# Optimization experiments

Hardware: AMD Instinct MI355X
Metric: run time of the kernel (lower is better)

The kernel has to match this reference:

```python
import jax, jax.numpy as jnp
import numpy as np

BN_EPS = 1e-5

def setup_inputs() -> dict:
    key = jax.random.key(0)
    k_x, k_w, k_g, k_b, k_p = jax.random.split(key, 5)
    N, Cin, H, W = 32, 128, 56, 56
    Cout, K = 256, 3
    x = jax.random.normal(k_x, (N, Cin, H, W), dtype=jnp.float32)
    # random spatial permutation (Dconv_rand's torch.randperm(H*W))
    perm = jax.random.permutation(k_p, H * W).astype(jnp.int32)
    # conv weight, kaiming-ish scale
    w = jax.random.normal(k_w, (Cout, Cin, K, K), dtype=jnp.float32) * (2.0 / (Cin * K * K)) ** 0.5
    gamma = jnp.ones((Cout,), dtype=jnp.float32)
    beta = jnp.zeros((Cout,), dtype=jnp.float32)
    return {"x": x, "w": w, "gamma": gamma, "beta": beta, "perm": perm}


def reference(x, w, gamma, beta, perm):
    N, C, H, W = x.shape
    # Dconv_rand: randomly permute spatial positions, then standard 3x3 conv
    xp = x.reshape(N, C, H * W)[:, :, perm].reshape(N, C, H, W)
    y = jax.lax.conv_general_dilated(
        xp, w,
        window_strides=(1, 1),
        padding=((1, 1), (1, 1)),
        dimension_numbers=("NCHW", "OIHW", "NCHW"),
    )  # [N, Cout, H, W]
    # BatchNorm2d (training-mode batch stats, biased variance, eps=1e-5)
    mean = jnp.mean(y, axis=(0, 2, 3), keepdims=True)
    var = jnp.mean((y - mean) ** 2, axis=(0, 2, 3), keepdims=True)
    y_hat = (y - mean) * jax.lax.rsqrt(var + BN_EPS)
    out = y_hat * gamma.reshape(1, -1, 1, 1) + beta.reshape(1, -1, 1, 1)
    return jnp.maximum(out, 0.0)  # ReLU
```

## Files before the change

kernel.cpp:

```cpp
#include <hip/hip_runtime.h>
#include <hip/hip_bf16.h>
#include <stdint.h>

typedef __attribute__((ext_vector_type(8))) short bf16x8;
typedef __attribute__((ext_vector_type(4))) float f32x4;

#define N_IMG 32
#define CIN 128
#define COUT 256
#define HH 56
#define HW (HH*HH)
#define HP 58
#define PXTOT (N_IMG*HW)
#define NT 36

#define XP_BYTES    27557888u
#define WT_BYTES    589824u
#define INV_BYTES   12544u
#define STATS_BYTES 2048u
#define WS_MIN      (XP_BYTES + WT_BYTES + INV_BYTES + STATS_BYTES)
#define Y_BYTES     51380224u

__device__ __forceinline__ unsigned short f2bf(float f) {
  unsigned int u = __builtin_bit_cast(unsigned int, f);
  unsigned int r = u + 0x7FFFu + ((u >> 16) & 1u);
  return (unsigned short)(r >> 16);
}
__device__ __forceinline__ float bf2f(unsigned short s) {
  return __builtin_bit_cast(float, (unsigned int)s << 16);
}
__device__ __forceinline__ void gload_lds16(const void* g, void* l) {
  __builtin_amdgcn_global_load_lds((const __attribute__((address_space(1))) void*)g,
                                   (__attribute__((address_space(3))) void*)l, 16, 0, 0);
}

#define BAR()    __builtin_amdgcn_s_barrier()
#define WAITV4() asm volatile("s_waitcnt vmcnt(4)" ::: "memory")
#define WAITV0() asm volatile("s_waitcnt vmcnt(0)" ::: "memory")
#define WAITL()  asm volatile("s_waitcnt lgkmcnt(0)" ::: "memory")
#define SCHEDB() __builtin_amdgcn_sched_barrier(0)

__global__ __launch_bounds__(256) void wcvt_kernel(const float* __restrict__ w,
                                                   unsigned short* __restrict__ wt,
                                                   const int* __restrict__ perm,
                                                   int* __restrict__ inv,
                                                   float* __restrict__ stats) {
  int i = blockIdx.x * 256 + threadIdx.x;
  if (i < HW) inv[perm[i]] = i;
  if (i < 512) stats[i] = 0.f;
  if (i >= NT * COUT * 32) return;
  int kk = i >> 13;
  int r = i & 8191;
  int co = r >> 5, cl = r & 31;
  int o = kk >> 2, cb = kk & 3;
  int c = cb * 32 + cl;
  wt[i] = f2bf(w[(co * CIN + c) * 9 + o]);
}

__global__ __launch_bounds__(256) void pad_perm_kernel(const float* __restrict__ x,
                                                       const int* __restrict__ inv,
                                                       unsigned short* __restrict__ xp) {
  __shared__ unsigned short T[64 * 128];
  __shared__ int dest_off[64];
  int b = blockIdx.x;
  int n = b / 49;
  int k = b % 49;
  int s0 = k * 64;
  int t = threadIdx.x;

  if (t < 160) {
    int pi = k * 5 + (t >> 5);
    if (pi < 228) {
      int h, w2;
      if (pi < 58)       { h = 0;            w2 = pi; }
      else if (pi < 116) { h = 57;           w2 = pi - 58; }
      else if (pi < 172) { h = pi - 116 + 1; w2 = 0; }
      else               { h = pi - 172 + 1; w2 = 57; }
      uint2 z = {0u, 0u};
      *(uint2*)(xp + (size_t)((n * HP + h) * HP + w2) * CIN + (t & 31) * 4) = z;
    }
  }

  if (t < 64) {
    int s = inv[s0 + t];
    int h = s / HH, w = s % HH;
    dest_off[t] = ((n * HP + h + 1) * HP + (w + 1)) * CIN;
  }
  const float* xplane = x + (size_t)n * CIN * HW;
  #pragma unroll
  for (int i = 0; i < 32; ++i) {
    int idx = i * 256 + t;
    int c = idx >> 6, j = idx & 63;
    float v = xplane[c * HW + s0 + j];
    int byte = j * 256 + ((2 * c) ^ ((j & 7) << 4));
    *(unsigned short*)((char*)T + byte) = f2bf(v);
  }
  __syncthreads();
  #pragma unroll
  for (int i = 0; i < 4; ++i) {
    int u = i * 256 + t;
    int j = u >> 4, chunk = u & 15;
    int byte = j * 256 + ((chunk * 16) ^ ((j & 7) << 4));
    bf16x8 v = *(const bf16x8*)((const char*)T + byte);
    *(bf16x8*)(xp + dest_off[j] + chunk * 8) = v;
  }
}

template<int YMODE>
__global__ __launch_bounds__(256, 2) void conv_kernel(const unsigned short* __restrict__ xp,
                                                      const unsigned short* __restrict__ wt,
                                                      unsigned short* __restrict__ ybf,
                                                      float* __restrict__ yf32,
                                                      float* __restrict__ stats) {
  extern __shared__ unsigned short lds[];
  int t = threadIdx.x;
  int lane = t & 63, wid = t >> 6;
  int l = lane & 15, g = lane >> 4;
  int phys = blockIdx.x;
  int b = (phys & 7) * 98 + (phys >> 3);
  int pT = b >> 1;
  int coT = b & 1;
  int p0 = pT * 256;

  int lg = ((lane & 3) - (lane >> 3)) & 3;
  int aoff[2], adst[2];
  #pragma unroll
  for (int i = 0; i < 2; ++i) {
    int r = (wid * 2 + i) * 16 + (lane >> 2);
    aoff[i] = r * 32 + lg * 8;
    adst[i] = (wid * 2 + i) * 512 + lane * 8;
  }
  int bsrc[4], bdst[4];
  #pragma unroll
  for (int i = 0; i < 4; ++i) {
    int r = (wid * 4 + i) * 16 + (lane >> 2);
    int px = p0 + r;
    int n = px / HW, s = px % HW;
    int hi = s / HH, wi = s % HH;
    bsrc[i] = ((n * HP + hi) * HP + wi) * CIN + lg * 8;
    bdst[i] = (wid * 4 + i) * 512 + lane * 8;
  }
  const unsigned short* wbase = wt + coT * 128 * 32;

  auto stageA = [&](int kt) {
    const unsigned short* s0 = wbase + kt * 8192;
    unsigned short* d = lds + (kt & 1) * 4096;
    gload_lds16(s0 + aoff[0], d + adst[0]);
    gload_lds16(s0 + aoff[1], d + adst[1]);
  };
  auto stageB = [&](int kt, int buf) {
    int o = kt >> 2, cb = kt & 3;
    int koff = ((o / 3) * HP + (o % 3)) * CIN + cb * 32;
    unsigned short* d = lds + 8192 + buf * 8192;
    #pragma unroll
    for (int i = 0; i < 4; ++i)
      gload_lds16(xp + bsrc[i] + koff, d + bdst[i]);
  };

  int pcs = ((g + (l >> 1)) & 3) * 8;
  int arow = l * 32 + pcs;
  int brow = (wid * 64 + l) * 32 + pcs;

  bf16x8 afr[8], bfr[4];
  f32x4 acc[8][4];
  #pragma unroll
  for (int m = 0; m < 8; ++m)
    #pragma unroll
    for (int n = 0; n < 4; ++n) acc[m][n] = (f32x4)0.f;

#define LDA_ALL { _Pragma("unroll") for (int mm = 0; mm < 8; ++mm) \
    afr[mm] = *(const bf16x8*)(curA + arow + mm * 16 * 32); }
#define LDB_ALL { _Pragma("unroll") for (int nn = 0; nn < 4; ++nn) \
    bfr[nn] = *(const bf16x8*)(curB + brow + nn * 16 * 32); }
#define MFMA_ALL { _Pragma("unroll") for (int mm = 0; mm < 8; ++mm) \
    _Pragma("unroll") for (int nn = 0; nn < 4; ++nn) \
      acc[mm][nn] = __builtin_amdgcn_mfma_f32_16x16x32_bf16(afr[mm], bfr[nn], acc[mm][nn], 0, 0, 0); }

  stageA(0);
  stageB(0, 0);
  stageB(1, 1);
  WAITV4();
  BAR();

  int pb = 0;
  #pragma unroll 1
  for (int kt = 0; kt < NT; ++kt) {
    const unsigned short* curA = lds + (kt & 1) * 4096;
    const unsigned short* curB = lds + 8192 + pb * 8192;
    bool st1 = (kt + 1) < NT;
    bool st2 = (kt + 2) < NT;
    int pb2 = pb + 2; if (pb2 >= 3) pb2 -= 3;
    LDA_ALL; LDB_ALL;
    if (st1) stageA(kt + 1);
    if (st2) stageB(kt + 2, pb2);
    BAR();
    WAITL(); SCHEDB();
    __builtin_amdgcn_s_setprio(1);
    MFMA_ALL;
    __builtin_amdgcn_s_setprio(0);
    if (st2) { WAITV4(); } else if (st1) { WAITV0(); }
    BAR();
    pb = (pb + 1 == 3) ? 0 : pb + 1;
  }
#undef LDA_ALL
#undef LDB_ALL
#undef MFMA_ALL

  float ps1[8][4], ps2[8][4];
  #pragma unroll
  for (int m = 0; m < 8; ++m)
    #pragma unroll
    for (int j = 0; j < 4; ++j) {
      float a = 0.f, b2 = 0.f;
      #pragma unroll
      for (int n = 0; n < 4; ++n) { float v = acc[m][n][j]; a += v; b2 += v * v; }
      #pragma unroll
      for (int off = 1; off < 16; off <<= 1) {
        a  += __shfl_xor(a, off, 64);
        b2 += __shfl_xor(b2, off, 64);
      }
      ps1[m][j] = a; ps2[m][j] = b2;
    }

  #pragma unroll
  for (int n = 0; n < 4; ++n) {
    int px = p0 + wid * 64 + n * 16 + l;
    if (YMODE == 1) {
      #pragma unroll
      for (int m = 0; m < 8; ++m) {
        int co = coT * 128 + m * 16 + g * 4;
        #pragma unroll
        for (int j = 0; j < 4; ++j)
          ybf[(size_t)(co + j) * PXTOT + px] = f2bf(acc[m][n][j]);
      }
    } else {
      int nimg = px / HW, s = px % HW;
      float* obase = yf32 + (size_t)nimg * COUT * HW + s;
      #pragma unroll
      for (int m = 0; m < 8; ++m) {
        int co = coT * 128 + m * 16 + g * 4;
        #pragma unroll
        for (int j = 0; j < 4; ++j)
          obase[(size_t)(co + j) * HW] = acc[m][n][j];
      }
    }
  }

  float* sb = (float*)lds;
  if (l == 0) {
    #pragma unroll
    for (int m = 0; m < 8; ++m)
      #pragma unroll
      for (int j = 0; j < 4; ++j) {
        int cl = m * 16 + g * 4 + j;
        sb[cl * 4 + wid] = ps1[m][j];
        sb[512 + cl * 4 + wid] = ps2[m][j];
      }
  }
  BAR();
  if (t < 128) {
    int co = coT * 128 + t;
    float a  = sb[t * 4] + sb[t * 4 + 1] + sb[t * 4 + 2] + sb[t * 4 + 3];
    float b2 = sb[512 + t * 4] + sb[512 + t * 4 + 1] + sb[512 + t * 4 + 2] + sb[512 + t * 4 + 3];
    atomicAdd(&stats[co], a);
    atomicAdd(&stats[256 + co], b2);
  }
}

__global__ __launch_bounds__(256) void bnrelu1_kernel(const unsigned short* __restrict__ y,
                                                      const float* __restrict__ stats,
                                                      const float* __restrict__ gamma,
                                                      const float* __restrict__ beta,
                                                      float* __restrict__ out) {
  int idx = blockIdx.x * 256 + threadIdx.x;
  const int UN = PXTOT / 8;
  int co = idx / UN;
  int rem = idx - co * UN;
  float cnt = (float)PXTOT;
  float mean = stats[co] / cnt;
  float var = stats[256 + co] / cnt - mean * mean;
  float sc = gamma[co] * rsqrtf(var + 1e-5f);
  float sh = beta[co] - mean * sc;
  bf16x8 v = *(const bf16x8*)(y + (size_t)co * PXTOT + rem * 8);
  int px0 = rem * 8;
  int n = px0 / HW, s = px0 - n * HW;
  float* o = out + ((size_t)n * COUT + co) * HW + s;
  float4 r0, r1;
  r0.x = fmaxf(bf2f((unsigned short)v[0]) * sc + sh, 0.f);
  r0.y = fmaxf(bf2f((unsigned short)v[1]) * sc + sh, 0.f);
  r0.z = fmaxf(bf2f((unsigned short)v[2]) * sc + sh, 0.f);
  r0.w = fmaxf(bf2f((unsigned short)v[3]) * sc + sh, 0.f);
  r1.x = fmaxf(bf2f((unsigned short)v[4]) * sc + sh, 0.f);
  r1.y = fmaxf(bf2f((unsigned short)v[5]) * sc + sh, 0.f);
  r1.z = fmaxf(bf2f((unsigned short)v[6]) * sc + sh, 0.f);
  r1.w = fmaxf(bf2f((unsigned short)v[7]) * sc + sh, 0.f);
  ((float4*)o)[0] = r0;
  ((float4*)o)[1] = r1;
}

__global__ __launch_bounds__(256) void bnrelu0_kernel(float* __restrict__ y,
                                                      const float* __restrict__ stats,
                                                      const float* __restrict__ gamma,
                                                      const float* __restrict__ beta) {
  int idx = blockIdx.x * 256 + threadIdx.x;
  int plane = idx / (HW / 4);
  int co = plane & 255;
  float cnt = (float)PXTOT;
  float mean = stats[co] / cnt;
  float var = stats[256 + co] / cnt - mean * mean;
  float sc = gamma[co] * rsqrtf(var + 1e-5f);
  float sh = beta[co] - mean * sc;
  float4 v = ((float4*)y)[idx];
  v.x = fmaxf(v.x * sc + sh, 0.f);
  v.y = fmaxf(v.y * sc + sh, 0.f);
  v.z = fmaxf(v.z * sc + sh, 0.f);
  v.w = fmaxf(v.w * sc + sh, 0.f);
  ((float4*)y)[idx] = v;
}

extern "C" void kernel_launch(void* const* d_in, const int* in_sizes, int n_in,
                              void* d_out, int out_size, void* d_ws, size_t ws_size,
                              hipStream_t stream) {
  const float* x     = (const float*)d_in[0];
  const float* w     = (const float*)d_in[1];
  const float* gamma = (const float*)d_in[2];
  const float* beta  = (const float*)d_in[3];
  const int*   perm  = (const int*)d_in[4];
  float* out = (float*)d_out;
  char* ws = (char*)d_ws;

  unsigned short* xp = (unsigned short*)ws;
  unsigned short* wt = (unsigned short*)(ws + XP_BYTES);
  int* inv           = (int*)(ws + XP_BYTES + WT_BYTES);
  float* stats       = (float*)(ws + XP_BYTES + WT_BYTES + INV_BYTES);
  unsigned short* y  = (unsigned short*)(ws + WS_MIN);
  bool ymode = ws_size >= (size_t)WS_MIN + Y_BYTES;

  hipFuncSetAttribute(reinterpret_cast<const void*>(conv_kernel<1>),
                      hipFuncAttributeMaxDynamicSharedMemorySize, 65536);
  hipFuncSetAttribute(reinterpret_cast<const void*>(conv_kernel<0>),
                      hipFuncAttributeMaxDynamicSharedMemorySize, 65536);

  wcvt_kernel<<<1152, 256, 0, stream>>>(w, wt, perm, inv, stats);
  pad_perm_kernel<<<N_IMG * 49, 256, 0, stream>>>(x, inv, xp);
  if (ymode) {
    conv_kernel<1><<<784, 256, 65536, stream>>>(xp, wt, y, out, stats);
    bnrelu1_kernel<<<COUT * (PXTOT / 8) / 256, 256, 0, stream>>>(y, stats, gamma, beta, out);
  } else {
    conv_kernel<0><<<784, 256, 65536, stream>>>(xp, wt, (unsigned short*)out, out, stats);
    bnrelu0_kernel<<<N_IMG * COUT * HW / 4 / 256, 256, 0, stream>>>(out, stats, gamma, beta);
  }
}
```

Before: 121.9 us.

## Shrink conv tile to 128x128 with 2x2 wave layout and static LDS

The conv block tile drops from 128 channels x 256 pixels to 128x128, with the four waves arranged 2x2 instead of splitting only along pixels. The grid doubles to 1568 blocks, LDS usage falls to 40KB static, and per-thread accumulators halve, which should allow more resident blocks and better load balance across CUs. In exchange, each block reuses its loaded data less: weight tiles are reloaded twice as often, and the arithmetic intensity per LDS byte drops.

```diff
diff --git a/kernel.cpp b/kernel.cpp
--- a/kernel.cpp
+++ b/kernel.cpp
@@ -35,7 +35,7 @@
 }
 
 #define BAR()    __builtin_amdgcn_s_barrier()
-#define WAITV4() asm volatile("s_waitcnt vmcnt(4)" ::: "memory")
+#define WAITV2() asm volatile("s_waitcnt vmcnt(2)" ::: "memory")
 #define WAITV0() asm volatile("s_waitcnt vmcnt(0)" ::: "memory")
 #define WAITL()  asm volatile("s_waitcnt lgkmcnt(0)" ::: "memory")
 #define SCHEDB() __builtin_amdgcn_sched_barrier(0)
@@ -112,33 +112,30 @@
                                                       unsigned short* __restrict__ ybf,
                                                       float* __restrict__ yf32,
                                                       float* __restrict__ stats) {
-  extern __shared__ unsigned short lds[];
+  __shared__ __align__(16) unsigned short lds[20480];
   int t = threadIdx.x;
   int lane = t & 63, wid = t >> 6;
+  int wm = wid >> 1, wn = wid & 1;
   int l = lane & 15, g = lane >> 4;
   int phys = blockIdx.x;
-  int b = (phys & 7) * 98 + (phys >> 3);
+  int b = (phys & 7) * 196 + (phys >> 3);
   int pT = b >> 1;
   int coT = b & 1;
-  int p0 = pT * 256;
+  int p0 = pT * 128;
 
   int lg = ((lane & 3) - (lane >> 3)) & 3;
   int aoff[2], adst[2];
+  int bsrc[2], bdst[2];
   #pragma unroll
   for (int i = 0; i < 2; ++i) {
     int r = (wid * 2 + i) * 16 + (lane >> 2);
     aoff[i] = r * 32 + lg * 8;
     adst[i] = (wid * 2 + i) * 512 + lane * 8;
-  }
-  int bsrc[4], bdst[4];
-  #pragma unroll
-  for (int i = 0; i < 4; ++i) {
-    int r = (wid * 4 + i) * 16 + (lane >> 2);
     int px = p0 + r;
     int n = px / HW, s = px % HW;
     int hi = s / HH, wi = s % HH;
     bsrc[i] = ((n * HP + hi) * HP + wi) * CIN + lg * 8;
-    bdst[i] = (wid * 4 + i) * 512 + lane * 8;
+    bdst[i] = adst[i];
   }
   const unsigned short* wbase = wt + coT * 128 * 32;
 
@@ -151,42 +148,41 @@
   auto stageB = [&](int kt, int buf) {
     int o = kt >> 2, cb = kt & 3;
     int koff = ((o / 3) * HP + (o % 3)) * CIN + cb * 32;
-    unsigned short* d = lds + 8192 + buf * 8192;
-    #pragma unroll
-    for (int i = 0; i < 4; ++i)
-      gload_lds16(xp + bsrc[i] + koff, d + bdst[i]);
+    unsigned short* d = lds + 8192 + buf * 4096;
+    gload_lds16(xp + bsrc[0] + koff, d + bdst[0]);
+    gload_lds16(xp + bsrc[1] + koff, d + bdst[1]);
   };
 
   int pcs = ((g + (l >> 1)) & 3) * 8;
-  int arow = l * 32 + pcs;
-  int brow = (wid * 64 + l) * 32 + pcs;
-
-  bf16x8 afr[8], bfr[4];
-  f32x4 acc[8][4];
-  #pragma unroll
-  for (int m = 0; m < 8; ++m)
+  int arow = (wm * 64 + l) * 32 + pcs;
+  int brow = (wn * 64 + l) * 32 + pcs;
+
+  bf16x8 afr[4], bfr[4];
+  f32x4 acc[4][4];
+  #pragma unroll
+  for (int m = 0; m < 4; ++m)
     #pragma unroll
     for (int n = 0; n < 4; ++n) acc[m][n] = (f32x4)0.f;
 
-#define LDA_ALL { _Pragma("unroll") for (int mm = 0; mm < 8; ++mm) \
+#define LDA_ALL { _Pragma("unroll") for (int mm = 0; mm < 4; ++mm) \
     afr[mm] = *(const bf16x8*)(curA + arow + mm * 16 * 32); }
 #define LDB_ALL { _Pragma("unroll") for (int nn = 0; nn < 4; ++nn) \
     bfr[nn] = *(const bf16x8*)(curB + brow + nn * 16 * 32); }
-#define MFMA_ALL { _Pragma("unroll") for (int mm = 0; mm < 8; ++mm) \
+#define MFMA_ALL { _Pragma("unroll") for (int mm = 0; mm < 4; ++mm) \
     _Pragma("unroll") for (int nn = 0; nn < 4; ++nn) \
       acc[mm][nn] = __builtin_amdgcn_mfma_f32_16x16x32_bf16(afr[mm], bfr[nn], acc[mm][nn], 0, 0, 0); }
 
   stageA(0);
   stageB(0, 0);
   stageB(1, 1);
-  WAITV4();
+  WAITV2();
   BAR();
 
   int pb = 0;
   #pragma unroll 1
   for (int kt = 0; kt < NT; ++kt) {
     const unsigned short* curA = lds + (kt & 1) * 4096;
-    const unsigned short* curB = lds + 8192 + pb * 8192;
+    const unsigned short* curB = lds + 8192 + pb * 4096;
     bool st1 = (kt + 1) < NT;
     bool st2 = (kt + 2) < NT;
     int pb2 = pb + 2; if (pb2 >= 3) pb2 -= 3;
@@ -198,7 +194,7 @@
     __builtin_amdgcn_s_setprio(1);
     MFMA_ALL;
     __builtin_amdgcn_s_setprio(0);
-    if (st2) { WAITV4(); } else if (st1) { WAITV0(); }
+    if (st2) { WAITV2(); } else if (st1) { WAITV0(); }
     BAR();
     pb = (pb + 1 == 3) ? 0 : pb + 1;
   }
@@ -206,9 +202,9 @@
 #undef LDB_ALL
 #undef MFMA_ALL
 
-  float ps1[8][4], ps2[8][4];
-  #pragma unroll
-  for (int m = 0; m < 8; ++m)
+  float ps1[4][4], ps2[4][4];
+  #pragma unroll
+  for (int m = 0; m < 4; ++m)
     #pragma unroll
     for (int j = 0; j < 4; ++j) {
       float a = 0.f, b2 = 0.f;
@@ -224,11 +220,11 @@
 
   #pragma unroll
   for (int n = 0; n < 4; ++n) {
-    int px = p0 + wid * 64 + n * 16 + l;
+    int px = p0 + wn * 64 + n * 16 + l;
     if (YMODE == 1) {
       #pragma unroll
-      for (int m = 0; m < 8; ++m) {
-        int co = coT * 128 + m * 16 + g * 4;
+      for (int m = 0; m < 4; ++m) {
+        int co = coT * 128 + wm * 64 + m * 16 + g * 4;
         #pragma unroll
         for (int j = 0; j < 4; ++j)
           ybf[(size_t)(co + j) * PXTOT + px] = f2bf(acc[m][n][j]);
@@ -237,8 +233,8 @@
       int nimg = px / HW, s = px % HW;
       float* obase = yf32 + (size_t)nimg * COUT * HW + s;
       #pragma unroll
-      for (int m = 0; m < 8; ++m) {
-        int co = coT * 128 + m * 16 + g * 4;
+      for (int m = 0; m < 4; ++m) {
+        int co = coT * 128 + wm * 64 + m * 16 + g * 4;
         #pragma unroll
         for (int j = 0; j < 4; ++j)
           obase[(size_t)(co + j) * HW] = acc[m][n][j];
@@ -249,21 +245,19 @@
   float* sb = (float*)lds;
   if (l == 0) {
     #pragma unroll
-    for (int m = 0; m < 8; ++m)
+    for (int m = 0; m < 4; ++m)
       #pragma unroll
       for (int j = 0; j < 4; ++j) {
-        int cl = m * 16 + g * 4 + j;
-        sb[cl * 4 + wid] = ps1[m][j];
-        sb[512 + cl * 4 + wid] = ps2[m][j];
+        int cl = wm * 64 + m * 16 + g * 4 + j;
+        sb[cl * 2 + wn] = ps1[m][j];
+        sb[256 + cl * 2 + wn] = ps2[m][j];
       }
   }
   BAR();
   if (t < 128) {
     int co = coT * 128 + t;
-    float a  = sb[t * 4] + sb[t * 4 + 1] + sb[t * 4 + 2] + sb[t * 4 + 3];
-    float b2 = sb[512 + t * 4] + sb[512 + t * 4 + 1] + sb[512 + t * 4 + 2] + sb[512 + t * 4 + 3];
-    atomicAdd(&stats[co], a);
-    atomicAdd(&stats[256 + co], b2);
+    atomicAdd(&stats[co],       sb[t * 2] + sb[t * 2 + 1]);
+    atomicAdd(&stats[256 + co], sb[256 + t * 2] + sb[256 + t * 2 + 1]);
   }
 }
 
@@ -336,18 +330,13 @@
   unsigned short* y  = (unsigned short*)(ws + WS_MIN);
   bool ymode = ws_size >= (size_t)WS_MIN + Y_BYTES;
 
-  hipFuncSetAttribute(reinterpret_cast<const void*>(conv_kernel<1>),
-                      hipFuncAttributeMaxDynamicSharedMemorySize, 65536);
-  hipFuncSetAttribute(reinterpret_cast<const void*>(conv_kernel<0>),
-                      hipFuncAttributeMaxDynamicSharedMemorySize, 65536);
-
   wcvt_kernel<<<1152, 256, 0, stream>>>(w, wt, perm, inv, stats);
   pad_perm_kernel<<<N_IMG * 49, 256, 0, stream>>>(x, inv, xp);
   if (ymode) {
-    conv_kernel<1><<<784, 256, 65536, stream>>>(xp, wt, y, out, stats);
+    conv_kernel<1><<<1568, 256, 0, stream>>>(xp, wt, y, out, stats);
     bnrelu1_kernel<<<COUT * (PXTOT / 8) / 256, 256, 0, stream>>>(y, stats, gamma, beta, out);
   } else {
-    conv_kernel<0><<<784, 256, 65536, stream>>>(xp, wt, (unsigned short*)out, out, stats);
+    conv_kernel<0><<<1568, 256, 0, stream>>>(xp, wt, (unsigned short*)out, out, stats);
     bnrelu0_kernel<<<N_IMG * COUT * HW / 4 / 256, 256, 0, stream>>>(out, stats, gamma, beta);
   }
 }
```

New measurement: 136.3 us. 1.12x slower.
